# Optimization experiments

Hardware: AMD Instinct MI355X
Metric: run time of the kernel (lower is better)

Reference implementation:

```python
import jax, jax.numpy as jnp
import numpy as np
from jax import lax

I, H, C = 1086, 16, 15


def _lstm_layer(x, w_ih, w_hh, b):
    # x: [B, T, in], w_ih: [4H, in], w_hh: [4H, H], b: [4H]  (b = b_ih + b_hh)
    B = x.shape[0]
    Hd = w_hh.shape[1]
    # precompute the big input projection outside the scan
    pre = jnp.einsum('bti,gi->btg', x, w_ih) + b  # [B, T, 4H]

    def step(carry, pt):
        h, c = carry
        gates = pt + h @ w_hh.T  # [B, 4H]
        i, f, g, o = jnp.split(gates, 4, axis=-1)  # torch gate order i,f,g,o
        i = jax.nn.sigmoid(i)
        f = jax.nn.sigmoid(f)
        g = jnp.tanh(g)
        o = jax.nn.sigmoid(o)
        c = f * c + i * g
        h = o * jnp.tanh(c)
        return (h, c), h

    h0 = jnp.zeros((B, Hd), x.dtype)
    c0 = jnp.zeros((B, Hd), x.dtype)
    _, ys = lax.scan(step, (h0, c0), jnp.swapaxes(pre, 0, 1))
    return jnp.swapaxes(ys, 0, 1)  # [B, T, H]


def setup_inputs() -> dict:
    key = jax.random.key(0)
    ks = jax.random.split(key, 20)
    s = 1.0 / np.sqrt(H)  # torch LSTM/Linear default init scale
    x = jax.random.normal(ks[0], (256, 200, I), dtype=jnp.float32)

    def w(k, shape):
        return jax.random.uniform(k, shape, jnp.float32, -s, s)

    inp = {'x': x}
    ins = [I, H, H, H]  # lstm1 layer0/1, lstm2 layer0/1
    names = ['l0a', 'l0b', 'l1a', 'l1b']
    ki = 1
    for n, d_in in zip(names, ins):
        inp['w_ih_' + n] = w(ks[ki], (4 * H, d_in)); ki += 1
        inp['w_hh_' + n] = w(ks[ki], (4 * H, H)); ki += 1
        inp['b_' + n] = w(ks[ki], (4 * H,)); ki += 1
    inp['w_fc1'] = w(ks[ki], (H, H)); ki += 1
    inp['b_fc1'] = w(ks[ki], (H,)); ki += 1
    inp['w_fc2'] = w(ks[ki], (C, H)); ki += 1
    inp['b_fc2'] = w(ks[ki], (C,))
    return inp


def reference(x, w_ih_l0a, w_hh_l0a, b_l0a, w_ih_l0b, w_hh_l0b, b_l0b,
              w_ih_l1a, w_hh_l1a, b_l1a, w_ih_l1b, w_hh_l1b, b_l1b,
              w_fc1, b_fc1, w_fc2, b_fc2):
    # lstm1 (2 layers), dropout between layers is identity in eval mode
    out = _lstm_layer(x, w_ih_l0a, w_hh_l0a, b_l0a)
    out = _lstm_layer(out, w_ih_l0b, w_hh_l0b, b_l0b)
    # lstm2 (2 layers)
    out = _lstm_layer(out, w_ih_l1a, w_hh_l1a, b_l1a)
    out = _lstm_layer(out, w_ih_l1b, w_hh_l1b, b_l1b)
    h_last = out[:, -1, :]  # [B, H]
    h = jax.nn.relu(h_last @ w_fc1.T + b_fc1)
    logits = h @ w_fc2.T + b_fc2  # [B, C]
    return jax.nn.softmax(logits, axis=1)
```

## Files before the change

kernel.cpp:

```cpp
#include <hip/hip_runtime.h>

#define T_STEPS 200
#define IN_DIM 1086
#define KTILES 34
#define M_TOTAL 51200

using f32x4v  = __attribute__((ext_vector_type(4))) float;
using bf16x8  = __attribute__((ext_vector_type(8))) short;
using u32x4   = __attribute__((ext_vector_type(4))) unsigned int;
using ushort8 = __attribute__((ext_vector_type(8))) unsigned short;
typedef unsigned uv2 __attribute__((ext_vector_type(2)));

#if __has_builtin(__builtin_amdgcn_permlane16_swap) && __has_builtin(__builtin_amdgcn_permlane32_swap)
#define HAVE_PERMLANE_SWAP 1
#else
#define HAVE_PERMLANE_SWAP 0
#endif

#if __has_builtin(__builtin_amdgcn_exp2f)
#define EXP2F(x) __builtin_amdgcn_exp2f(x)
#else
#define EXP2F(x) exp2f(x)
#endif

__device__ __forceinline__ float rl_f(float v, int lane) {
    return __uint_as_float((unsigned)__builtin_amdgcn_readlane((int)__float_as_uint(v), lane));
}

__global__ __launch_bounds__(256) void prepack_w(
    const float* __restrict__ W,
    unsigned short* __restrict__ Wh, unsigned short* __restrict__ Wl)
{
    int idx = blockIdx.x * 256 + threadIdx.x;
    if (idx >= KTILES * 4 * 64 * 8) return;
    int j = idx & 7;
    int n = (idx >> 3) & 63;
    int k = (idx >> 9) * 8 + j;
    float v = (k < IN_DIM) ? W[n * IN_DIM + k] : 0.0f;
    unsigned u = __float_as_uint(v);
    unsigned hi = u & 0xffff0000u;
    float lo = v - __uint_as_float(hi);
    Wh[idx] = (unsigned short)(u >> 16);
    Wl[idx] = (unsigned short)(__float_as_uint(lo) >> 16);
}

__device__ __forceinline__ void cvt_hilo(const float (&a)[8], bf16x8& hv, bf16x8& lv) {
    union { u32x4 u; bf16x8 v; } H, L;
    #pragma unroll
    for (int p = 0; p < 4; ++p) {
        float a0 = a[2 * p], a1 = a[2 * p + 1];
        unsigned u0 = __float_as_uint(a0), u1 = __float_as_uint(a1);
        unsigned h0 = u0 & 0xffff0000u, h1 = u1 & 0xffff0000u;
        H.u[p] = (u0 >> 16) | h1;
        float l0 = a0 - __uint_as_float(h0);
        float l1 = a1 - __uint_as_float(h1);
        L.u[p] = (__float_as_uint(l0) >> 16) | (__float_as_uint(l1) & 0xffff0000u);
    }
    hv = H.v; lv = L.v;
}

__global__ __launch_bounds__(256) void pre0_gemm_v3(
    const float* __restrict__ X,
    const unsigned short* __restrict__ Wh, const unsigned short* __restrict__ Wl,
    const float* __restrict__ bias, float* __restrict__ out)
{
    __shared__ float As[64 * 32];
    __shared__ unsigned short BsH[2048];
    __shared__ unsigned short BsL[2048];

    const int tid  = threadIdx.x;
    const int lane = tid & 63;
    const int wv   = tid >> 6;
    const int fr   = lane & 15;
    const int kg   = lane >> 4;
    const long m0  = (long)blockIdx.x * 64;

    const int row0 = tid >> 4;
    const int cch  = (tid >> 1) & 7;
    const int half = tid & 1;
    const int ldsA0 = row0 * 128 + ((cch ^ (row0 & 7)) << 4) + half * 8;
    const bool tailskip = (tid & 15) == 15;
    const float* xsrc = X + (m0 + row0) * (long)IN_DIM + (tid & 15) * 2;
    char* aB = (char*)As;

    f32x4v acc[4];
    #pragma unroll
    for (int nf = 0; nf < 4; ++nf)
        #pragma unroll
        for (int r = 0; r < 4; ++r) acc[nf][r] = 0.0f;

    for (int kt = 0; kt < KTILES; ++kt) {
        const bool tail = (kt == KTILES - 1);
        __syncthreads();

        float2 av[4];
        #pragma unroll
        for (int i = 0; i < 4; ++i) {
            float2 v;
            if (tail && tailskip) { v.x = 0.0f; v.y = 0.0f; }
            else v = *(const float2*)(xsrc + (long)i * 16 * IN_DIM + kt * 32);
            av[i] = v;
        }
        ushort8 bhv = *(const ushort8*)(Wh + kt * 2048 + tid * 8);
        ushort8 blv = *(const ushort8*)(Wl + kt * 2048 + tid * 8);
        #pragma unroll
        for (int i = 0; i < 4; ++i)
            *(float2*)(aB + ldsA0 + i * 2048) = av[i];
        *(ushort8*)(BsH + tid * 8) = bhv;
        *(ushort8*)(BsL + tid * 8) = blv;
        __syncthreads();

        const int r = wv * 16 + fr;
        const int s = fr & 7;
        const float* pa1 = As + r * 32 + ((((2 * kg)    ) ^ s) << 2);
        const float* pa2 = As + r * 32 + ((((2 * kg) | 1) ^ s) << 2);
        float a[8];
        *(f32x4v*)&a[0] = *(const f32x4v*)pa1;
        *(f32x4v*)&a[4] = *(const f32x4v*)pa2;
        bf16x8 ah, al;
        cvt_hilo(a, ah, al);
        bf16x8 bh[4], bl[4];
        #pragma unroll
        for (int nf = 0; nf < 4; ++nf) {
            bh[nf] = *(const bf16x8*)(BsH + (kg * 64 + nf * 16 + fr) * 8);
            bl[nf] = *(const bf16x8*)(BsL + (kg * 64 + nf * 16 + fr) * 8);
        }
        #pragma unroll
        for (int nf = 0; nf < 4; ++nf) {
            acc[nf] = __builtin_amdgcn_mfma_f32_16x16x32_bf16(ah, bh[nf], acc[nf], 0, 0, 0);
            acc[nf] = __builtin_amdgcn_mfma_f32_16x16x32_bf16(al, bh[nf], acc[nf], 0, 0, 0);
            acc[nf] = __builtin_amdgcn_mfma_f32_16x16x32_bf16(ah, bl[nf], acc[nf], 0, 0, 0);
        }
    }

    float bvv[4];
    #pragma unroll
    for (int nf = 0; nf < 4; ++nf) bvv[nf] = bias[nf * 16 + fr];
    #pragma unroll
    for (int nf = 0; nf < 4; ++nf)
        #pragma unroll
        for (int rr = 0; rr < 4; ++rr) {
            long row = m0 + wv * 16 + kg * 4 + rr;
            out[row * 64 + nf * 16 + fr] = acc[nf][rr] + bvv[nf];
        }
}

__global__ __launch_bounds__(256) void mega_scan(
    const float* __restrict__ pre0, const float* __restrict__ whh0,
    const float* __restrict__ wih1, const float* __restrict__ whh1, const float* __restrict__ b1,
    const float* __restrict__ wih2, const float* __restrict__ whh2, const float* __restrict__ b2,
    const float* __restrict__ wih3, const float* __restrict__ whh3, const float* __restrict__ b3,
    const float* __restrict__ w_fc1, const float* __restrict__ b_fc1,
    const float* __restrict__ w_fc2, const float* __restrict__ b_fc2,
    float* __restrict__ out)
{
    __shared__ float buf[3][T_STEPS][16];

    const int b    = blockIdx.x;
    const int tid  = threadIdx.x;
    const int g    = tid & 63;
    const int wv   = tid >> 6;

    bool sel16 = false, sel32 = false;
#if HAVE_PERMLANE_SWAP
    {
        uv2 q16 = __builtin_amdgcn_permlane16_swap((unsigned)g, (unsigned)g, false, false);
        sel16 = (__builtin_amdgcn_readfirstlane((int)q16[1]) == 16);
        uv2 q32 = __builtin_amdgcn_permlane32_swap((unsigned)g, (unsigned)g, false, false);
        sel32 = (__builtin_amdgcn_readfirstlane((int)q32[1]) == 32);
    }
#endif

    const float* wih = nullptr; const float* whh; const float* bias = nullptr;
    if      (wv == 0) { whh = whh0; }
    else if (wv == 1) { wih = wih1; whh = whh1; bias = b1; }
    else if (wv == 2) { wih = wih2; whh = whh2; bias = b2; }
    else              { wih = wih3; whh = whh3; bias = b3; }

    float whh_r[16];
    #pragma unroll
    for (int q = 0; q < 4; ++q)
        *(float4*)&whh_r[q * 4] = *(const float4*)&whh[g * 16 + q * 4];
    float wih_r[16]; float bg = 0.0f;
    if (wv) {
        #pragma unroll
        for (int q = 0; q < 4; ++q)
            *(float4*)&wih_r[q * 4] = *(const float4*)&wih[g * 16 + q * 4];
        bg = bias[g];
    }

    const float* pb = pre0 + (long)b * T_STEPS * 64 + g;
    float pc = 0.0f, p1 = 0.0f, p2 = 0.0f;
    if (wv == 0) { pc = pb[0]; p1 = pb[64]; p2 = pb[128]; }

    float hs[16];
    #pragma unroll
    for (int k = 0; k < 16; ++k) hs[k] = 0.0f;
    float c = 0.0f;

    const int q4 = g >> 4;
    const float escale = (q4 == 2) ? -2.8853900817779268f : -1.4426950408889634f;
    const float am = (q4 == 2) ? 2.0f : 1.0f;
    const float aa = (q4 == 2) ? -1.0f : 0.0f;

    for (int tau = 0; tau < T_STEPS + 3; ++tau) {
        __syncthreads();
        const int t = tau - wv;
        if (t >= 0 && t < T_STEPS) {
            float xr[16];
            if (wv) {
                #pragma unroll
                for (int q = 0; q < 4; ++q)
                    *(float4*)&xr[q * 4] = *(const float4*)&buf[wv - 1][t][q * 4];
            }
            float r0 = fmaf(whh_r[0], hs[0], wv ? bg : pc);
            float r1 = whh_r[1] * hs[1];
            float r2 = whh_r[2] * hs[2];
            float r3 = whh_r[3] * hs[3];
            #pragma unroll
            for (int k = 4; k < 16; k += 4) {
                r0 = fmaf(whh_r[k + 0], hs[k + 0], r0);
                r1 = fmaf(whh_r[k + 1], hs[k + 1], r1);
                r2 = fmaf(whh_r[k + 2], hs[k + 2], r2);
                r3 = fmaf(whh_r[k + 3], hs[k + 3], r3);
            }
            float acc = (r0 + r1) + (r2 + r3);
            if (wv) {
                float p0 = wih_r[0] * xr[0];
                float q1 = wih_r[1] * xr[1];
                float q2 = wih_r[2] * xr[2];
                float q3 = wih_r[3] * xr[3];
                #pragma unroll
                for (int k = 4; k < 16; k += 4) {
                    p0 = fmaf(wih_r[k + 0], xr[k + 0], p0);
                    q1 = fmaf(wih_r[k + 1], xr[k + 1], q1);
                    q2 = fmaf(wih_r[k + 2], xr[k + 2], q2);
                    q3 = fmaf(wih_r[k + 3], xr[k + 3], q3);
                }
                acc += (p0 + q1) + (q2 + q3);
            }
            float e = EXP2F(escale * acc);
            float s = __builtin_amdgcn_rcpf(1.0f + e);
            float a = fmaf(am, s, aa);
#if HAVE_PERMLANE_SWAP
            unsigned au = __float_as_uint(a);
            uv2 r16 = __builtin_amdgcn_permlane16_swap(au, au, false, false);
            uv2 r32 = __builtin_amdgcn_permlane32_swap(au, au, false, false);
            unsigned fvu = sel16 ? r16[1] : r16[0];
            unsigned gvu = sel32 ? r32[1] : r32[0];
            uv2 r48 = __builtin_amdgcn_permlane16_swap(gvu, gvu, false, false);
            unsigned ovu = sel16 ? r48[1] : r48[0];
            float fv = __uint_as_float(fvu);
            float gv = __uint_as_float(gvu);
            float ov = __uint_as_float(ovu);
#else
            float fv = __shfl_xor(a, 16, 64);
            float gv = __shfl_xor(a, 32, 64);
            float ov = __shfl_xor(a, 48, 64);
#endif
            c = fmaf(fv, c, a * gv);
            float e2 = EXP2F(-2.8853900817779268f * c);
            float s2 = __builtin_amdgcn_rcpf(1.0f + e2);
            float hn = fmaf(ov + ov, s2, -ov);
            if (wv < 3 && g < 16) buf[wv][t][g] = hn;
            #pragma unroll
            for (int k = 0; k < 16; ++k) hs[k] = rl_f(hn, k);
            if (wv == 0) {
                pc = p1; p1 = p2;
                int tn = t + 3; tn = tn < T_STEPS ? tn : T_STEPS - 1;
                p2 = pb[(long)tn * 64];
            }
        }
    }

    if (wv == 3 && g < 16) {
        float a1 = b_fc1[g];
        #pragma unroll
        for (int k = 0; k < 16; ++k) a1 = fmaf(w_fc1[g * 16 + k], hs[k], a1);
        a1 = fmaxf(a1, 0.0f);
        float h1[16];
        #pragma unroll
        for (int k = 0; k < 16; ++k) h1[k] = rl_f(a1, k);
        float lg = -3.0e38f;
        if (g < 15) {
            lg = b_fc2[g];
            #pragma unroll
            for (int k = 0; k < 16; ++k) lg = fmaf(w_fc2[g * 16 + k], h1[k], lg);
        }
        float mx = lg;
        #pragma unroll
        for (int d = 8; d >= 1; d >>= 1) mx = fmaxf(mx, __shfl_xor(mx, d, 16));
        float ev = (g < 15) ? EXP2F(1.4426950408889634f * (lg - mx)) : 0.0f;
        float sm = ev;
        #pragma unroll
        for (int d = 8; d >= 1; d >>= 1) sm += __shfl_xor(sm, d, 16);
        if (g < 15) out[b * 15 + g] = ev * __builtin_amdgcn_rcpf(sm);
    }
}

extern "C" void kernel_launch(void* const* d_in, const int* in_sizes, int n_in,
                              void* d_out, int out_size, void* d_ws, size_t ws_size,
                              hipStream_t stream) {
    const float* x    = (const float*)d_in[0];
    const float* wih0 = (const float*)d_in[1];
    const float* whh0 = (const float*)d_in[2];
    const float* b0   = (const float*)d_in[3];
    const float* wih1 = (const float*)d_in[4];
    const float* whh1 = (const float*)d_in[5];
    const float* b1   = (const float*)d_in[6];
    const float* wih2 = (const float*)d_in[7];
    const float* whh2 = (const float*)d_in[8];
    const float* b2   = (const float*)d_in[9];
    const float* wih3 = (const float*)d_in[10];
    const float* whh3 = (const float*)d_in[11];
    const float* b3   = (const float*)d_in[12];
    const float* wfc1 = (const float*)d_in[13];
    const float* bfc1 = (const float*)d_in[14];
    const float* wfc2 = (const float*)d_in[15];
    const float* bfc2 = (const float*)d_in[16];

    float* pre0 = (float*)d_ws;
    unsigned short* Wh = (unsigned short*)((char*)d_ws + 13107200);
    unsigned short* Wl = (unsigned short*)((char*)d_ws + 13107200 + 139264);

    prepack_w<<<dim3((KTILES * 4 * 64 * 8 + 255) / 256), dim3(256), 0, stream>>>(wih0, Wh, Wl);
    pre0_gemm_v3<<<dim3(M_TOTAL / 64), dim3(256), 0, stream>>>(x, Wh, Wl, b0, pre0);
    mega_scan<<<dim3(256), dim3(256), 0, stream>>>(pre0, whh0,
        wih1, whh1, b1, wih2, whh2, b2, wih3, whh3, b3,
        wfc1, bfc1, wfc2, bfc2, (float*)d_out);
}
```

Baseline: 162.5 us.

## Stage full 16-row X panel in LDS once and stream weights from global

```diff
diff --git a/kernel.cpp b/kernel.cpp
--- a/kernel.cpp
+++ b/kernel.cpp
@@ -4,11 +4,11 @@
 #define IN_DIM 1086
 #define KTILES 34
 #define M_TOTAL 51200
+#define ROWPAD 1100
 
 using f32x4v  = __attribute__((ext_vector_type(4))) float;
 using bf16x8  = __attribute__((ext_vector_type(8))) short;
 using u32x4   = __attribute__((ext_vector_type(4))) unsigned int;
-using ushort8 = __attribute__((ext_vector_type(8))) unsigned short;
 typedef unsigned uv2 __attribute__((ext_vector_type(2)));
 
 #if __has_builtin(__builtin_amdgcn_permlane16_swap) && __has_builtin(__builtin_amdgcn_permlane32_swap)
@@ -59,90 +59,69 @@
     hv = H.v; lv = L.v;
 }
 
-__global__ __launch_bounds__(256) void pre0_gemm_v3(
+__global__ __launch_bounds__(256) void pre0_gemm_v4(
     const float* __restrict__ X,
     const unsigned short* __restrict__ Wh, const unsigned short* __restrict__ Wl,
     const float* __restrict__ bias, float* __restrict__ out)
 {
-    __shared__ float As[64 * 32];
-    __shared__ unsigned short BsH[2048];
-    __shared__ unsigned short BsL[2048];
-
-    const int tid  = threadIdx.x;
-    const int lane = tid & 63;
-    const int wv   = tid >> 6;
-    const int fr   = lane & 15;
-    const int kg   = lane >> 4;
-    const long m0  = (long)blockIdx.x * 64;
-
-    const int row0 = tid >> 4;
-    const int cch  = (tid >> 1) & 7;
-    const int half = tid & 1;
-    const int ldsA0 = row0 * 128 + ((cch ^ (row0 & 7)) << 4) + half * 8;
-    const bool tailskip = (tid & 15) == 15;
-    const float* xsrc = X + (m0 + row0) * (long)IN_DIM + (tid & 15) * 2;
-    char* aB = (char*)As;
-
-    f32x4v acc[4];
-    #pragma unroll
-    for (int nf = 0; nf < 4; ++nf)
-        #pragma unroll
-        for (int r = 0; r < 4; ++r) acc[nf][r] = 0.0f;
+    __shared__ float As[16 * ROWPAD];
+
+    const int tid = threadIdx.x;
+    const long m0 = (long)blockIdx.x * 16;
+
+    const float* src = X + m0 * IN_DIM;
+    float4 v[17];
+    #pragma unroll
+    for (int p = 0; p < 17; ++p) {
+        int idx = tid + p * 256;
+        if (idx < 4344) v[p] = *(const float4*)(src + idx * 4);
+    }
+    if (tid < 112) {
+        int r = tid / 7, cc = tid - r * 7;
+        *(float2*)&As[r * ROWPAD + 1086 + cc * 2] = float2{0.0f, 0.0f};
+    }
+    #pragma unroll
+    for (int p = 0; p < 17; ++p) {
+        int idx = tid + p * 256;
+        if (idx < 4344) {
+            int f2 = idx * 2;
+            int r0 = f2 / 543,       c0 = f2 - r0 * 543;
+            int r1 = (f2 + 1) / 543, c1 = (f2 + 1) - r1 * 543;
+            *(float2*)&As[r0 * ROWPAD + c0 * 2] = float2{v[p].x, v[p].y};
+            *(float2*)&As[r1 * ROWPAD + c1 * 2] = float2{v[p].z, v[p].w};
+        }
+    }
+    __syncthreads();
+
+    const int fr = tid & 15;
+    const int kg = (tid >> 4) & 3;
+    const int wv = tid >> 6;
+
+    f32x4v acc;
+    #pragma unroll
+    for (int r = 0; r < 4; ++r) acc[r] = 0.0f;
 
     for (int kt = 0; kt < KTILES; ++kt) {
-        const bool tail = (kt == KTILES - 1);
-        __syncthreads();
-
-        float2 av[4];
-        #pragma unroll
-        for (int i = 0; i < 4; ++i) {
-            float2 v;
-            if (tail && tailskip) { v.x = 0.0f; v.y = 0.0f; }
-            else v = *(const float2*)(xsrc + (long)i * 16 * IN_DIM + kt * 32);
-            av[i] = v;
-        }
-        ushort8 bhv = *(const ushort8*)(Wh + kt * 2048 + tid * 8);
-        ushort8 blv = *(const ushort8*)(Wl + kt * 2048 + tid * 8);
-        #pragma unroll
-        for (int i = 0; i < 4; ++i)
-            *(float2*)(aB + ldsA0 + i * 2048) = av[i];
-        *(ushort8*)(BsH + tid * 8) = bhv;
-        *(ushort8*)(BsL + tid * 8) = blv;
-        __syncthreads();
-
-        const int r = wv * 16 + fr;
-        const int s = fr & 7;
-        const float* pa1 = As + r * 32 + ((((2 * kg)    ) ^ s) << 2);
-        const float* pa2 = As + r * 32 + ((((2 * kg) | 1) ^ s) << 2);
+        const float* pa = As + fr * ROWPAD + kt * 32 + kg * 8;
         float a[8];
-        *(f32x4v*)&a[0] = *(const f32x4v*)pa1;
-        *(f32x4v*)&a[4] = *(const f32x4v*)pa2;
+        *(f32x4v*)&a[0] = *(const f32x4v*)pa;
+        *(f32x4v*)&a[4] = *(const f32x4v*)(pa + 4);
         bf16x8 ah, al;
         cvt_hilo(a, ah, al);
-        bf16x8 bh[4], bl[4];
-        #pragma unroll
-        for (int nf = 0; nf < 4; ++nf) {
-            bh[nf] = *(const bf16x8*)(BsH + (kg * 64 + nf * 16 + fr) * 8);
-            bl[nf] = *(const bf16x8*)(BsL + (kg * 64 + nf * 16 + fr) * 8);
-        }
-        #pragma unroll
-        for (int nf = 0; nf < 4; ++nf) {
-            acc[nf] = __builtin_amdgcn_mfma_f32_16x16x32_bf16(ah, bh[nf], acc[nf], 0, 0, 0);
-            acc[nf] = __builtin_amdgcn_mfma_f32_16x16x32_bf16(al, bh[nf], acc[nf], 0, 0, 0);
-            acc[nf] = __builtin_amdgcn_mfma_f32_16x16x32_bf16(ah, bl[nf], acc[nf], 0, 0, 0);
-        }
-    }
-
-    float bvv[4];
-    #pragma unroll
-    for (int nf = 0; nf < 4; ++nf) bvv[nf] = bias[nf * 16 + fr];
-    #pragma unroll
-    for (int nf = 0; nf < 4; ++nf)
-        #pragma unroll
-        for (int rr = 0; rr < 4; ++rr) {
-            long row = m0 + wv * 16 + kg * 4 + rr;
-            out[row * 64 + nf * 16 + fr] = acc[nf][rr] + bvv[nf];
-        }
+        const long bbase = (long)kt * 2048 + (kg * 64 + wv * 16 + fr) * 8;
+        bf16x8 bh = *(const bf16x8*)(Wh + bbase);
+        bf16x8 bl = *(const bf16x8*)(Wl + bbase);
+        acc = __builtin_amdgcn_mfma_f32_16x16x32_bf16(ah, bh, acc, 0, 0, 0);
+        acc = __builtin_amdgcn_mfma_f32_16x16x32_bf16(al, bh, acc, 0, 0, 0);
+        acc = __builtin_amdgcn_mfma_f32_16x16x32_bf16(ah, bl, acc, 0, 0, 0);
+    }
+
+    const float bv = bias[wv * 16 + fr];
+    #pragma unroll
+    for (int r = 0; r < 4; ++r) {
+        long row = m0 + kg * 4 + r;
+        out[row * 64 + wv * 16 + fr] = acc[r] + bv;
+    }
 }
 
 __global__ __launch_bounds__(256) void mega_scan(
@@ -324,7 +303,7 @@
     unsigned short* Wl = (unsigned short*)((char*)d_ws + 13107200 + 139264);
 
     prepack_w<<<dim3((KTILES * 4 * 64 * 8 + 255) / 256), dim3(256), 0, stream>>>(wih0, Wh, Wl);
-    pre0_gemm_v3<<<dim3(M_TOTAL / 64), dim3(256), 0, stream>>>(x, Wh, Wl, b0, pre0);
+    pre0_gemm_v4<<<dim3(M_TOTAL / 16), dim3(256), 0, stream>>>(x, Wh, Wl, b0, pre0);
     mega_scan<<<dim3(256), dim3(256), 0, stream>>>(pre0, whh0,
         wih1, whh1, b1, wih2, whh2, b2, wih3, whh3, b3,
         wfc1, bfc1, wfc2, bfc2, (float*)d_out);
```

After: 183.2 us. 12.7% more time.

## Double-buffer input GEMM tiles with direct global-to-LDS loads

Applied to the files above, without the earlier changes.

```diff
diff --git a/kernel.cpp b/kernel.cpp
--- a/kernel.cpp
+++ b/kernel.cpp
@@ -8,7 +8,6 @@
 using f32x4v  = __attribute__((ext_vector_type(4))) float;
 using bf16x8  = __attribute__((ext_vector_type(8))) short;
 using u32x4   = __attribute__((ext_vector_type(4))) unsigned int;
-using ushort8 = __attribute__((ext_vector_type(8))) unsigned short;
 typedef unsigned uv2 __attribute__((ext_vector_type(2)));
 
 #if __has_builtin(__builtin_amdgcn_permlane16_swap) && __has_builtin(__builtin_amdgcn_permlane32_swap)
@@ -22,6 +21,10 @@
 #else
 #define EXP2F(x) exp2f(x)
 #endif
+
+#define GLDS(gp, lp, sz) __builtin_amdgcn_global_load_lds(                         \
+    (const __attribute__((address_space(1))) unsigned int*)(gp),                   \
+    (__attribute__((address_space(3))) unsigned int*)(lp), sz, 0, 0)
 
 __device__ __forceinline__ float rl_f(float v, int lane) {
     return __uint_as_float((unsigned)__builtin_amdgcn_readlane((int)__float_as_uint(v), lane));
@@ -59,14 +62,13 @@
     hv = H.v; lv = L.v;
 }
 
-__global__ __launch_bounds__(256) void pre0_gemm_v3(
+__global__ __launch_bounds__(256) void pre0_gemm_v5(
     const float* __restrict__ X,
     const unsigned short* __restrict__ Wh, const unsigned short* __restrict__ Wl,
     const float* __restrict__ bias, float* __restrict__ out)
 {
-    __shared__ float As[64 * 32];
-    __shared__ unsigned short BsH[2048];
-    __shared__ unsigned short BsL[2048];
+    __shared__ float          As[2][2048];
+    __shared__ unsigned short Bs[2][2][2048];
 
     const int tid  = threadIdx.x;
     const int lane = tid & 63;
@@ -75,13 +77,14 @@
     const int kg   = lane >> 4;
     const long m0  = (long)blockIdx.x * 64;
 
-    const int row0 = tid >> 4;
-    const int cch  = (tid >> 1) & 7;
-    const int half = tid & 1;
-    const int ldsA0 = row0 * 128 + ((cch ^ (row0 & 7)) << 4) + half * 8;
-    const bool tailskip = (tid & 15) == 15;
-    const float* xsrc = X + (m0 + row0) * (long)IN_DIM + (tid & 15) * 2;
-    char* aB = (char*)As;
+    const int rbase = wv * 16 + (lane >> 5);
+    const int sidx  = (lane >> 2) & 7;
+    const int dsub  = lane & 3;
+    int koff[8];
+    #pragma unroll
+    for (int i = 0; i < 8; ++i)
+        koff[i] = ((sidx ^ ((rbase + 2 * i) & 7)) * 4 + dsub) * 4;
+    const char* Xrow = (const char*)X + (m0 + rbase) * 4344;
 
     f32x4v acc[4];
     #pragma unroll
@@ -89,47 +92,49 @@
         #pragma unroll
         for (int r = 0; r < 4; ++r) acc[nf][r] = 0.0f;
 
+    {
+        #pragma unroll
+        for (int i = 0; i < 8; ++i) {
+            int off = koff[i];
+            GLDS(Xrow + (long)i * 8688 + off, &As[0][wv * 512 + i * 64], 4);
+        }
+        GLDS(Wh + tid * 8, (char*)Bs[0][0] + wv * 1024, 16);
+        GLDS(Wl + tid * 8, (char*)Bs[0][1] + wv * 1024, 16);
+    }
+
     for (int kt = 0; kt < KTILES; ++kt) {
-        const bool tail = (kt == KTILES - 1);
+        const int cur = kt & 1;
         __syncthreads();
 
-        float2 av[4];
-        #pragma unroll
-        for (int i = 0; i < 4; ++i) {
-            float2 v;
-            if (tail && tailskip) { v.x = 0.0f; v.y = 0.0f; }
-            else v = *(const float2*)(xsrc + (long)i * 16 * IN_DIM + kt * 32);
-            av[i] = v;
-        }
-        ushort8 bhv = *(const ushort8*)(Wh + kt * 2048 + tid * 8);
-        ushort8 blv = *(const ushort8*)(Wl + kt * 2048 + tid * 8);
-        #pragma unroll
-        for (int i = 0; i < 4; ++i)
-            *(float2*)(aB + ldsA0 + i * 2048) = av[i];
-        *(ushort8*)(BsH + tid * 8) = bhv;
-        *(ushort8*)(BsL + tid * 8) = blv;
-        __syncthreads();
-
-        const int r = wv * 16 + fr;
-        const int s = fr & 7;
-        const float* pa1 = As + r * 32 + ((((2 * kg)    ) ^ s) << 2);
-        const float* pa2 = As + r * 32 + ((((2 * kg) | 1) ^ s) << 2);
+        if (kt + 1 < KTILES) {
+            const int nb = cur ^ 1, kb = (kt + 1) * 128;
+            #pragma unroll
+            for (int i = 0; i < 8; ++i) {
+                int off = kb + koff[i];
+                off = off > 4340 ? 4340 : off;
+                GLDS(Xrow + (long)i * 8688 + off, &As[nb][wv * 512 + i * 64], 4);
+            }
+            GLDS(Wh + (size_t)(kt + 1) * 2048 + tid * 8, (char*)Bs[nb][0] + wv * 1024, 16);
+            GLDS(Wl + (size_t)(kt + 1) * 2048 + tid * 8, (char*)Bs[nb][1] + wv * 1024, 16);
+        }
+
+        const int r  = wv * 16 + fr;
+        const int r7 = r & 7;
+        const float* pa1 = &As[cur][r * 32 + (((2 * kg) ^ r7) << 2)];
+        const float* pa2 = &As[cur][r * 32 + ((((2 * kg) | 1) ^ r7) << 2)];
         float a[8];
         *(f32x4v*)&a[0] = *(const f32x4v*)pa1;
         *(f32x4v*)&a[4] = *(const f32x4v*)pa2;
         bf16x8 ah, al;
         cvt_hilo(a, ah, al);
-        bf16x8 bh[4], bl[4];
         #pragma unroll
         for (int nf = 0; nf < 4; ++nf) {
-            bh[nf] = *(const bf16x8*)(BsH + (kg * 64 + nf * 16 + fr) * 8);
-            bl[nf] = *(const bf16x8*)(BsL + (kg * 64 + nf * 16 + fr) * 8);
-        }
-        #pragma unroll
-        for (int nf = 0; nf < 4; ++nf) {
-            acc[nf] = __builtin_amdgcn_mfma_f32_16x16x32_bf16(ah, bh[nf], acc[nf], 0, 0, 0);
-            acc[nf] = __builtin_amdgcn_mfma_f32_16x16x32_bf16(al, bh[nf], acc[nf], 0, 0, 0);
-            acc[nf] = __builtin_amdgcn_mfma_f32_16x16x32_bf16(ah, bl[nf], acc[nf], 0, 0, 0);
+            const int bofs = (kg * 64 + nf * 16 + fr) * 8;
+            bf16x8 bh = *(const bf16x8*)&Bs[cur][0][bofs];
+            bf16x8 bl = *(const bf16x8*)&Bs[cur][1][bofs];
+            acc[nf] = __builtin_amdgcn_mfma_f32_16x16x32_bf16(ah, bh, acc[nf], 0, 0, 0);
+            acc[nf] = __builtin_amdgcn_mfma_f32_16x16x32_bf16(al, bh, acc[nf], 0, 0, 0);
+            acc[nf] = __builtin_amdgcn_mfma_f32_16x16x32_bf16(ah, bl, acc[nf], 0, 0, 0);
         }
     }
 
@@ -189,7 +194,7 @@
         bg = bias[g];
     }
 
-    const float* pb = pre0 + (long)b * T_STEPS * 64 + g;
+    const float* pb = pre0 + (size_t)b * T_STEPS * 64 + g;
     float pc = 0.0f, p1 = 0.0f, p2 = 0.0f;
     if (wv == 0) { pc = pb[0]; p1 = pb[64]; p2 = pb[128]; }
 
@@ -268,7 +273,7 @@
             if (wv == 0) {
                 pc = p1; p1 = p2;
                 int tn = t + 3; tn = tn < T_STEPS ? tn : T_STEPS - 1;
-                p2 = pb[(long)tn * 64];
+                p2 = pb[(size_t)tn * 64];
             }
         }
     }
@@ -324,7 +329,7 @@
     unsigned short* Wl = (unsigned short*)((char*)d_ws + 13107200 + 139264);
 
     prepack_w<<<dim3((KTILES * 4 * 64 * 8 + 255) / 256), dim3(256), 0, stream>>>(wih0, Wh, Wl);
-    pre0_gemm_v3<<<dim3(M_TOTAL / 64), dim3(256), 0, stream>>>(x, Wh, Wl, b0, pre0);
+    pre0_gemm_v5<<<dim3(M_TOTAL / 64), dim3(256), 0, stream>>>(x, Wh, Wl, b0, pre0);
     mega_scan<<<dim3(256), dim3(256), 0, stream>>>(pre0, whh0,
         wih1, whh1, b1, wih2, whh2, b2, wih3, whh3, b3,
         wfc1, bfc1, wfc2, bfc2, (float*)d_out);
```

New measurement: 167.1 us. 2.8% more time.
